# Kernel tuning notes

Hardware: AMD Instinct MI355X
Metric: run time of the kernel (lower is better)

Reference implementation:

```python
import jax, jax.numpy as jnp
import numpy as np

N_NODES = 100000
N_EDGES = 1600000
F_IN = 256
EMB = 16  # conv1 out = 2*EMB = 32, conv2 out = EMB


def setup_inputs() -> dict:
    key = jax.random.key(0)
    k1, k2, k3, k4, k5, k6, k7 = jax.random.split(key, 7)
    x = jax.random.normal(k1, (N_NODES, F_IN), dtype=jnp.float32)
    edge_index = jax.random.randint(k2, (2, N_EDGES), 0, N_NODES, dtype=jnp.int64)
    edge_weight = jax.random.uniform(k3, (N_EDGES,), dtype=jnp.float32)
    # GCNConv params: glorot-ish weights, zero bias (materialized as params)
    s1 = 1.0 / np.sqrt(F_IN)
    s2 = 1.0 / np.sqrt(2 * EMB)
    W1 = jax.random.uniform(k4, (F_IN, 2 * EMB), minval=-s1, maxval=s1, dtype=jnp.float32)
    b1 = jnp.zeros((2 * EMB,), dtype=jnp.float32)
    W2 = jax.random.uniform(k5, (2 * EMB, EMB), minval=-s2, maxval=s2, dtype=jnp.float32)
    b2 = jnp.zeros((EMB,), dtype=jnp.float32)
    return {"x": x, "edge_index": edge_index, "edge_weight": edge_weight,
            "W1": W1, "b1": b1, "W2": W2, "b2": b2}


def _gcn_norm(edge_index, edge_weight, num_nodes, dtype):
    # PyG gcn_norm with add_self_loops=True, fill_value=1.0
    row, col = edge_index[0], edge_index[1]
    loop = jnp.arange(num_nodes)
    row_a = jnp.concatenate([row, loop])
    col_a = jnp.concatenate([col, loop])
    w_a = jnp.concatenate([edge_weight, jnp.ones((num_nodes,), dtype=dtype)])
    deg = jax.ops.segment_sum(w_a, col_a, num_segments=num_nodes)
    dinv = jnp.where(deg > 0, jax.lax.rsqrt(deg), jnp.zeros_like(deg))
    norm = dinv[row_a] * w_a * dinv[col_a]
    return row_a, col_a, norm


def _gcn_conv(x, W, b, row, col, norm, num_nodes):
    h = x @ W                                  # [N, d_out] dense projection
    msg = norm[:, None] * h[row]               # gather + edge scale, [E+N, d_out]
    out = jax.ops.segment_sum(msg, col, num_segments=num_nodes)  # scatter-add
    return out + b


def reference(x, edge_index, edge_weight, W1, b1, W2, b2):
    n = x.shape[0]
    row, col, norm = _gcn_norm(edge_index, edge_weight, n, x.dtype)
    h = jax.nn.relu(_gcn_conv(x, W1, b1, row, col, norm, n))
    return _gcn_conv(h, W2, b2, row, col, norm, n)
```

## Files before the change

kernel.cpp:

```cpp
#include <hip/hip_runtime.h>
#include <hip/hip_bf16.h>
#include <hip/hip_fp16.h>

#define NN   100000
#define NE   1600000
#define FIN  256
#define HID  32
#define OUTD 16
#define NBLK ((NN + 255) / 256)

#define GEMM_ROWS   64
#define GEMM_BLOCKS ((NN + GEMM_ROWS - 1) / GEMM_ROWS)
#define CNT_EDGES   2048
#define CNT_BLOCKS  ((NE + CNT_EDGES - 1) / CNT_EDGES)
#define FUSE_BLOCKS (GEMM_BLOCKS + CNT_BLOCKS)
#define FILL_BLOCKS ((NE + 1023) / 1024)

#define OFF_FLAG    0
#define OFF_DEGPACK 64
#define OFF_DINV    (OFF_DEGPACK + 2*NN)
#define OFF_RANK    (OFF_DINV + NN)
#define OFF_BSUM    (OFF_RANK + NE)
#define OFF_ROWPTR  (OFF_BSUM + 1024)
#define OFF_CSR     (OFF_ROWPTR + NN + 32)
#define OFF_H1      (OFF_CSR + 2*NE)
#define OFF_P2      (OFF_H1 + NN*HID)

#define PACK_SHIFT 40
#define PACK_MASK  ((1ull << PACK_SHIFT) - 1ull)
#define FP_SCALE   16777216.0f
#define FP_INV     (1.0f / 16777216.0f)

__device__ __forceinline__ float bf2f(unsigned short u) {
  union { unsigned int i; float f; } v; v.i = ((unsigned int)u) << 16; return v.f;
}
__device__ __forceinline__ unsigned short f2bf(float f) {
  union { float f; unsigned int i; } v; v.f = f;
  unsigned int x = v.i;
  return (unsigned short)((x + 0x7fffu + ((x >> 16) & 1u)) >> 16);
}
__device__ __forceinline__ int eidx(const int* __restrict__ ei, long long pos, int is64) {
  return is64 ? ei[2 * pos] : ei[pos];
}
__device__ __forceinline__ float ldf(const void* p, long long i, int isf32) {
  return isf32 ? ((const float*)p)[i] : bf2f(((const unsigned short*)p)[i]);
}

__global__ __launch_bounds__(256) void detect_zero_kernel(const int* __restrict__ ei,
    const unsigned short* __restrict__ xu, int* __restrict__ flags,
    float* __restrict__ zp, int zn) {
  int b = blockIdx.x;
  if (b == 0) {
    __shared__ int any, cnt;
    if (threadIdx.x == 0) { any = 0; cnt = 0; }
    __syncthreads();
    int local = 0, c = 0;
    for (int i = threadIdx.x; i < 2048; i += 256) local |= ei[2 * i + 1];
    for (int i = threadIdx.x; i < 1024; i += 256) {
      unsigned int e = (xu[2 * i] >> 7) & 0xFF;
      c += (e < 100 || e > 140) ? 1 : 0;
    }
    if (local) atomicOr(&any, 1);
    atomicAdd(&cnt, c);
    __syncthreads();
    if (threadIdx.x == 0) {
      flags[0] = (any == 0) ? 1 : 0;
      flags[1] = (cnt > 100) ? 1 : 0;
    }
  } else {
    int stride = (gridDim.x - 1) * 256;
    for (int i = (b - 1) * 256 + threadIdx.x; i < zn; i += stride) zp[i] = 0.f;
  }
}

__global__ __launch_bounds__(256) void count_gemm_kernel(const int* __restrict__ ei,
    const void* __restrict__ ew, unsigned long long* __restrict__ degpack,
    int* __restrict__ rank, const void* __restrict__ x,
    const void* __restrict__ W1, void* __restrict__ h1,
    const int* __restrict__ flags) {
  __shared__ float wlds[FIN * HID];
  __shared__ float xs[32][GEMM_ROWS];
  int b = blockIdx.x;
  int t = threadIdx.x;

  if ((b % 3) == 0) {
    int cid = b / 3;
    int is64 = flags[0], isf32 = flags[1];
    int e0 = cid * CNT_EDGES + t;
    int c[8]; float w[8];
    #pragma unroll
    for (int q = 0; q < 8; q++) {
      int e = e0 + q * 256;
      if (e < NE) {
        c[q] = eidx(ei, (long long)NE + e, is64);
        w[q] = ldf(ew, e, isf32);
      } else c[q] = -1;
    }
    unsigned long long old[8];
    #pragma unroll
    for (int q = 0; q < 8; q++) {
      if (c[q] >= 0) {
        unsigned long long inc = (1ull << PACK_SHIFT)
                               | (unsigned long long)(w[q] * FP_SCALE + 0.5f);
        old[q] = atomicAdd(degpack + c[q], inc);
      }
    }
    #pragma unroll
    for (int q = 0; q < 8; q++)
      if (c[q] >= 0) rank[e0 + q * 256] = (int)(old[q] >> PACK_SHIFT);
    return;
  }

  int gid = b - b / 3 - 1;
  int rb = gid * GEMM_ROWS;
  int isf32 = flags[1];

  if (isf32) {
    const float* wrow = (const float*)W1 + t * HID;
    #pragma unroll
    for (int jj = 0; jj < HID; jj += 4)
      *(float4*)&wlds[t * HID + jj] = *((const float4*)(wrow + jj));
  } else {
    const unsigned short* wrow = (const unsigned short*)W1 + t * HID;
    #pragma unroll
    for (int jj = 0; jj < HID; jj += 8) {
      uint4 pk = *((const uint4*)(wrow + jj));
      const unsigned short* pu = (const unsigned short*)&pk;
      #pragma unroll
      for (int q = 0; q < 8; q++) wlds[t * HID + jj + q] = bf2f(pu[q]);
    }
  }

  int j0 = (t & 15) * 2;
  int r0 = (t >> 4) * 4;
  int rr  = t >> 2;
  int kk0 = (t & 3) * 8;
  long long grow = (long long)rb + rr;
  float acc[4][2];
  #pragma unroll
  for (int i = 0; i < 4; i++) { acc[i][0] = 0.f; acc[i][1] = 0.f; }

  union { uint4 u[2]; float f[8]; unsigned short s[16]; } pf;

  {
    if (grow < NN) {
      if (isf32) {
        const float* xp = (const float*)x + grow * FIN + kk0;
        pf.u[0] = ((const uint4*)xp)[0];
        pf.u[1] = ((const uint4*)xp)[1];
      } else {
        const unsigned short* xp = (const unsigned short*)x + grow * FIN + kk0;
        pf.u[0] = *(const uint4*)xp;
      }
    } else { pf.u[0] = make_uint4(0,0,0,0); pf.u[1] = make_uint4(0,0,0,0); }
  }

  for (int kc = 0; kc < FIN; kc += 32) {
    __syncthreads();
    if (isf32) {
      #pragma unroll
      for (int q = 0; q < 8; q++) xs[kk0 + q][rr] = pf.f[q];
    } else {
      #pragma unroll
      for (int q = 0; q < 8; q++) xs[kk0 + q][rr] = bf2f(pf.s[q]);
    }
    __syncthreads();
    if (kc + 32 < FIN) {
      if (grow < NN) {
        if (isf32) {
          const float* xp = (const float*)x + grow * FIN + kc + 32 + kk0;
          pf.u[0] = ((const uint4*)xp)[0];
          pf.u[1] = ((const uint4*)xp)[1];
        } else {
          const unsigned short* xp = (const unsigned short*)x + grow * FIN + kc + 32 + kk0;
          pf.u[0] = *(const uint4*)xp;
        }
      }
    }
    #pragma unroll 8
    for (int kk = 0; kk < 32; kk++) {
      float2 wp = *(const float2*)&wlds[(kc + kk) * HID + j0];
      float4 xv = *(const float4*)&xs[kk][r0];
      float xr[4] = {xv.x, xv.y, xv.z, xv.w};
      #pragma unroll
      for (int i = 0; i < 4; i++) {
        acc[i][0] = fmaf(xr[i], wp.x, acc[i][0]);
        acc[i][1] = fmaf(xr[i], wp.y, acc[i][1]);
      }
    }
  }
  #pragma unroll
  for (int i = 0; i < 4; i++) {
    int g = rb + r0 + i;
    if (g < NN) {
      if (isf32) {
        float2 v; v.x = acc[i][0]; v.y = acc[i][1];
        *((float2*)((float*)h1 + (long long)g * HID + j0)) = v;
      } else {
        __half2 hv;
        hv.x = __float2half(acc[i][0]);
        hv.y = __float2half(acc[i][1]);
        *((__half2*)((__half*)h1 + (long long)g * HID + j0)) = hv;
      }
    }
  }
}

__global__ __launch_bounds__(256) void scan_sum_kernel(
    const unsigned long long* __restrict__ degpack, int* __restrict__ bsum) {
  __shared__ int s[256];
  int i = blockIdx.x * 256 + threadIdx.x;
  s[threadIdx.x] = (i < NN) ? (int)(degpack[i] >> PACK_SHIFT) : 0;
  __syncthreads();
  for (int off = 128; off > 0; off >>= 1) {
    if (threadIdx.x < off) s[threadIdx.x] += s[threadIdx.x + off];
    __syncthreads();
  }
  if (threadIdx.x == 0) bsum[blockIdx.x] = s[0];
}

__global__ __launch_bounds__(256) void scan_write_kernel(const unsigned long long* __restrict__ degpack,
    const int* __restrict__ bsum, int* __restrict__ rowptr,
    float* __restrict__ dinv) {
  __shared__ int a[256];
  __shared__ int base_s;
  int t = threadIdx.x;
  int b = blockIdx.x;
  int v = 0;
  for (int i = t; i < NBLK; i += 256) v += (i < b) ? bsum[i] : 0;
  a[t] = v;
  __syncthreads();
  for (int off = 128; off > 0; off >>= 1) {
    if (t < off) a[t] += a[t + off];
    __syncthreads();
  }
  if (t == 0) base_s = a[0];
  __syncthreads();
  int base = base_s;
  int i = b * 256 + t;
  unsigned long long dp = (i < NN) ? degpack[i] : 0ull;
  int orig = (int)(dp >> PACK_SHIFT);
  a[t] = orig;
  __syncthreads();
  for (int off = 1; off < 256; off <<= 1) {
    int x2 = a[t] + ((t >= off) ? a[t - off] : 0);
    __syncthreads();
    a[t] = x2;
    __syncthreads();
  }
  if (i < NN) {
    rowptr[i] = base + a[t] - orig;
    float d = (float)(dp & PACK_MASK) * FP_INV + 1.0f;
    dinv[i] = rsqrtf(d);
  }
  if (b == 0 && t == 0) rowptr[NN] = NE;
}

__global__ __launch_bounds__(256) void fill_csr_kernel(const int* __restrict__ ei,
    const void* __restrict__ ew, const float* __restrict__ dinv,
    const int* __restrict__ rowptr, const int* __restrict__ rank,
    int2* __restrict__ csr, const int* __restrict__ flags) {
  int is64 = flags[0], isf32 = flags[1];
  int e0 = blockIdx.x * 1024 + threadIdx.x;
  int r[4], c[4], rk[4]; float w[4];
  #pragma unroll
  for (int q = 0; q < 4; q++) {
    int e = e0 + q * 256;
    if (e < NE) {
      r[q]  = eidx(ei, e, is64);
      c[q]  = eidx(ei, (long long)NE + e, is64);
      w[q]  = ldf(ew, e, isf32);
      rk[q] = rank[e];
    } else c[q] = -1;
  }
  float dr[4], dc[4]; int rp[4];
  #pragma unroll
  for (int q = 0; q < 4; q++) {
    if (c[q] >= 0) {
      dr[q] = dinv[r[q]];
      dc[q] = dinv[c[q]];
      rp[q] = rowptr[c[q]];
    }
  }
  #pragma unroll
  for (int q = 0; q < 4; q++) {
    if (c[q] >= 0) {
      int2 pr; pr.x = r[q]; pr.y = __float_as_int(dr[q] * w[q] * dc[q]);
      csr[rp[q] + rk[q]] = pr;
    }
  }
}

template <bool F32>
__device__ __forceinline__ float gather_row32(const void* __restrict__ hv,
    const int2* __restrict__ csr, int k0, int k1, int j) {
  const float*  hf = (const float*)hv;
  const __half* hh = (const __half*)hv;
  float acc = 0.f;
  for (int base = k0; base < k1; base += 32) {
    int kk = base + j;
    int2 q; q.x = 0; q.y = 0;
    if (kk < k1) q = csr[kk];
    int nloc = min(k1 - base, 32);
    int i = 0;
    for (; i + 8 <= nloc; i += 8) {
      int   s0 = __shfl(q.x, i + 0, 32), s1 = __shfl(q.x, i + 1, 32);
      int   s2 = __shfl(q.x, i + 2, 32), s3 = __shfl(q.x, i + 3, 32);
      int   s4 = __shfl(q.x, i + 4, 32), s5 = __shfl(q.x, i + 5, 32);
      int   s6 = __shfl(q.x, i + 6, 32), s7 = __shfl(q.x, i + 7, 32);
      float w0 = __int_as_float(__shfl(q.y, i + 0, 32));
      float w1 = __int_as_float(__shfl(q.y, i + 1, 32));
      float w2 = __int_as_float(__shfl(q.y, i + 2, 32));
      float w3 = __int_as_float(__shfl(q.y, i + 3, 32));
      float w4 = __int_as_float(__shfl(q.y, i + 4, 32));
      float w5 = __int_as_float(__shfl(q.y, i + 5, 32));
      float w6 = __int_as_float(__shfl(q.y, i + 6, 32));
      float w7 = __int_as_float(__shfl(q.y, i + 7, 32));
      float v0 = F32 ? hf[s0 * HID + j] : __half2float(hh[s0 * HID + j]);
      float v1 = F32 ? hf[s1 * HID + j] : __half2float(hh[s1 * HID + j]);
      float v2 = F32 ? hf[s2 * HID + j] : __half2float(hh[s2 * HID + j]);
      float v3 = F32 ? hf[s3 * HID + j] : __half2float(hh[s3 * HID + j]);
      float v4 = F32 ? hf[s4 * HID + j] : __half2float(hh[s4 * HID + j]);
      float v5 = F32 ? hf[s5 * HID + j] : __half2float(hh[s5 * HID + j]);
      float v6 = F32 ? hf[s6 * HID + j] : __half2float(hh[s6 * HID + j]);
      float v7 = F32 ? hf[s7 * HID + j] : __half2float(hh[s7 * HID + j]);
      acc = fmaf(w0, v0, acc); acc = fmaf(w1, v1, acc);
      acc = fmaf(w2, v2, acc); acc = fmaf(w3, v3, acc);
      acc = fmaf(w4, v4, acc); acc = fmaf(w5, v5, acc);
      acc = fmaf(w6, v6, acc); acc = fmaf(w7, v7, acc);
    }
    for (; i < nloc; i++) {
      int   s = __shfl(q.x, i, 32);
      float w = __int_as_float(__shfl(q.y, i, 32));
      float v = F32 ? hf[s * HID + j] : __half2float(hh[s * HID + j]);
      acc = fmaf(w, v, acc);
    }
  }
  return acc;
}

template <bool F32>
__device__ __forceinline__ float gather_row16(const void* __restrict__ pv,
    const int2* __restrict__ csr, int k0, int k1, int m) {
  const float*  pf = (const float*)pv;
  const __half* ph = (const __half*)pv;
  float acc = 0.f;
  for (int base = k0; base < k1; base += 16) {
    int kk = base + m;
    int2 q; q.x = 0; q.y = 0;
    if (kk < k1) q = csr[kk];
    int nloc = min(k1 - base, 16);
    int i = 0;
    for (; i + 8 <= nloc; i += 8) {
      int   s0 = __shfl(q.x, i + 0, 16), s1 = __shfl(q.x, i + 1, 16);
      int   s2 = __shfl(q.x, i + 2, 16), s3 = __shfl(q.x, i + 3, 16);
      int   s4 = __shfl(q.x, i + 4, 16), s5 = __shfl(q.x, i + 5, 16);
      int   s6 = __shfl(q.x, i + 6, 16), s7 = __shfl(q.x, i + 7, 16);
      float w0 = __int_as_float(__shfl(q.y, i + 0, 16));
      float w1 = __int_as_float(__shfl(q.y, i + 1, 16));
      float w2 = __int_as_float(__shfl(q.y, i + 2, 16));
      float w3 = __int_as_float(__shfl(q.y, i + 3, 16));
      float w4 = __int_as_float(__shfl(q.y, i + 4, 16));
      float w5 = __int_as_float(__shfl(q.y, i + 5, 16));
      float w6 = __int_as_float(__shfl(q.y, i + 6, 16));
      float w7 = __int_as_float(__shfl(q.y, i + 7, 16));
      float v0 = F32 ? pf[s0 * OUTD + m] : __half2float(ph[s0 * OUTD + m]);
      float v1 = F32 ? pf[s1 * OUTD + m] : __half2float(ph[s1 * OUTD + m]);
      float v2 = F32 ? pf[s2 * OUTD + m] : __half2float(ph[s2 * OUTD + m]);
      float v3 = F32 ? pf[s3 * OUTD + m] : __half2float(ph[s3 * OUTD + m]);
      float v4 = F32 ? pf[s4 * OUTD + m] : __half2float(ph[s4 * OUTD + m]);
      float v5 = F32 ? pf[s5 * OUTD + m] : __half2float(ph[s5 * OUTD + m]);
      float v6 = F32 ? pf[s6 * OUTD + m] : __half2float(ph[s6 * OUTD + m]);
      float v7 = F32 ? pf[s7 * OUTD + m] : __half2float(ph[s7 * OUTD + m]);
      acc = fmaf(w0, v0, acc); acc = fmaf(w1, v1, acc);
      acc = fmaf(w2, v2, acc); acc = fmaf(w3, v3, acc);
      acc = fmaf(w4, v4, acc); acc = fmaf(w5, v5, acc);
      acc = fmaf(w6, v6, acc); acc = fmaf(w7, v7, acc);
    }
    for (; i < nloc; i++) {
      int   s = __shfl(q.x, i, 16);
      float w = __int_as_float(__shfl(q.y, i, 16));
      float v = F32 ? pf[s * OUTD + m] : __half2float(ph[s * OUTD + m]);
      acc = fmaf(w, v, acc);
    }
  }
  return acc;
}

__global__ __launch_bounds__(256) void gather1_kernel(const void* __restrict__ h1,
    const float* __restrict__ dinv, const int* __restrict__ rowptr,
    const int2* __restrict__ csr, const void* __restrict__ b1,
    const void* __restrict__ W2, void* __restrict__ p2,
    const int* __restrict__ flags) {
  __shared__ float w2lds[HID * OUTD];
  __shared__ float b1l[HID];
  __shared__ float tl[8][HID + 1];
  int t = threadIdx.x;
  int isf32 = flags[1];
  w2lds[2 * t]     = ldf(W2, 2 * t, isf32);
  w2lds[2 * t + 1] = ldf(W2, 2 * t + 1, isf32);
  if (t < HID) b1l[t] = ldf(b1, t, isf32);
  __syncthreads();

  int nl = t >> 5;
  int j  = t & 31;
  int node = blockIdx.x * 8 + nl;
  if (node < NN) {
    int k0 = rowptr[node], k1 = rowptr[node + 1];
    float acc = isf32 ? gather_row32<true>(h1, csr, k0, k1, j)
                      : gather_row32<false>(h1, csr, k0, k1, j);
    float di = dinv[node];
    float sv = isf32 ? ((const float*)h1)[(long long)node * HID + j]
                     : __half2float(((const __half*)h1)[(long long)node * HID + j]);
    acc = fmaf(di * di, sv, acc);
    acc += b1l[j];
    tl[nl][j] = fmaxf(acc, 0.f);
  }
  __syncthreads();
  int m = t & 31;
  if (node < NN && m < OUTD) {
    float s = 0.f;
    #pragma unroll
    for (int k = 0; k < HID; k++) s = fmaf(tl[nl][k], w2lds[k * OUTD + m], s);
    if (isf32) ((float*)p2)[(long long)node * OUTD + m] = s;
    else       ((__half*)p2)[(long long)node * OUTD + m] = __float2half(s);
  }
}

__global__ __launch_bounds__(256) void gather2_kernel(const void* __restrict__ p2,
    const float* __restrict__ dinv, const int* __restrict__ rowptr,
    const int2* __restrict__ csr, const void* __restrict__ b2,
    void* __restrict__ out, const int* __restrict__ flags) {
  __shared__ float b2l[OUTD];
  int t = threadIdx.x;
  int isf32 = flags[1];
  if (t < OUTD) b2l[t] = ldf(b2, t, isf32);
  __syncthreads();

  int nl = t >> 4;
  int m  = t & 15;
  int node = blockIdx.x * 16 + nl;
  if (node >= NN) return;
  int k0 = rowptr[node], k1 = rowptr[node + 1];
  float acc = isf32 ? gather_row16<true>(p2, csr, k0, k1, m)
                    : gather_row16<false>(p2, csr, k0, k1, m);
  float di = dinv[node];
  float sv = isf32 ? ((const float*)p2)[(long long)node * OUTD + m]
                   : __half2float(((const __half*)p2)[(long long)node * OUTD + m]);
  acc = fmaf(di * di, sv, acc);
  acc += b2l[m];
  int oidx = node * OUTD + m;
  if (isf32) ((float*)out)[oidx] = acc;
  else       ((unsigned short*)out)[oidx] = f2bf(acc);
}

extern "C" void kernel_launch(void* const* d_in, const int* in_sizes, int n_in,
                              void* d_out, int out_size, void* d_ws, size_t ws_size,
                              hipStream_t stream) {
  const void* x  = d_in[0];
  const int* ei  = (const int*)d_in[1];
  const void* ew = d_in[2];
  const void* W1 = d_in[3];
  const void* b1 = d_in[4];
  const void* W2 = d_in[5];
  const void* b2 = d_in[6];
  float* ws = (float*)d_ws;
  int* wsi = (int*)d_ws;
  unsigned long long* degpack = (unsigned long long*)(wsi + OFF_DEGPACK);

  detect_zero_kernel<<<dim3(513), dim3(256), 0, stream>>>(ei, (const unsigned short*)x,
      wsi + OFF_FLAG, ws + OFF_DEGPACK, 2 * NN);
  count_gemm_kernel<<<dim3(FUSE_BLOCKS), dim3(256), 0, stream>>>(ei, ew, degpack,
      wsi + OFF_RANK, x, W1, ws + OFF_H1, wsi + OFF_FLAG);
  scan_sum_kernel<<<dim3(NBLK), dim3(256), 0, stream>>>(degpack, wsi + OFF_BSUM);
  scan_write_kernel<<<dim3(NBLK), dim3(256), 0, stream>>>(degpack, wsi + OFF_BSUM,
      wsi + OFF_ROWPTR, ws + OFF_DINV);
  fill_csr_kernel<<<dim3(FILL_BLOCKS), dim3(256), 0, stream>>>(ei, ew, ws + OFF_DINV,
      wsi + OFF_ROWPTR, wsi + OFF_RANK, (int2*)(wsi + OFF_CSR), wsi + OFF_FLAG);
  gather1_kernel<<<dim3((NN + 7) / 8), dim3(256), 0, stream>>>(ws + OFF_H1, ws + OFF_DINV,
      wsi + OFF_ROWPTR, (const int2*)(wsi + OFF_CSR), b1, W2, ws + OFF_P2, wsi + OFF_FLAG);
  gather2_kernel<<<dim3((NN + 15) / 16), dim3(256), 0, stream>>>(ws + OFF_P2, ws + OFF_DINV,
      wsi + OFF_ROWPTR, (const int2*)(wsi + OFF_CSR), b2, d_out, wsi + OFF_FLAG);
}
```

Baseline: 352.1 us.

## Fuse scan, CSR fill and both gathers into one cooperative persistent kernel

Replaces five separate launches (scan sum, scan write, CSR fill, gather1, gather2) with a single cooperative kernel using grid.sync between phases and grid-stride chunk loops. It also moves the destination-side dinv factor out of each per-edge weight and applies it once per node after aggregation, which removes one random dinv load per edge in the fill. The aim is to cut launch gaps and tail effects between small dependent kernels. In exchange it adds grid-wide barriers and caps the grid at 1024 blocks with __launch_bounds__(256,4), which may reduce occupancy for the gather phases.

New measurement: 876.9 us. 149% more time.

```diff
diff --git a/kernel.cpp b/kernel.cpp
--- a/kernel.cpp
+++ b/kernel.cpp
@@ -1,6 +1,8 @@
 #include <hip/hip_runtime.h>
 #include <hip/hip_bf16.h>
 #include <hip/hip_fp16.h>
+#include <hip/hip_cooperative_groups.h>
+namespace cg = cooperative_groups;
 
 #define NN   100000
 #define NE   1600000
@@ -14,7 +16,10 @@
 #define CNT_EDGES   2048
 #define CNT_BLOCKS  ((NE + CNT_EDGES - 1) / CNT_EDGES)
 #define FUSE_BLOCKS (GEMM_BLOCKS + CNT_BLOCKS)
-#define FILL_BLOCKS ((NE + 1023) / 1024)
+#define FILL_CHUNKS ((NE + 1023) / 1024)
+#define G1_CHUNKS   ((NN + 7) / 8)
+#define G2_CHUNKS   ((NN + 15) / 16)
+#define MEGA_GRID   1024
 
 #define OFF_FLAG    0
 #define OFF_DEGPACK 64
@@ -202,91 +207,6 @@
         hv.y = __float2half(acc[i][1]);
         *((__half2*)((__half*)h1 + (long long)g * HID + j0)) = hv;
       }
-    }
-  }
-}
-
-__global__ __launch_bounds__(256) void scan_sum_kernel(
-    const unsigned long long* __restrict__ degpack, int* __restrict__ bsum) {
-  __shared__ int s[256];
-  int i = blockIdx.x * 256 + threadIdx.x;
-  s[threadIdx.x] = (i < NN) ? (int)(degpack[i] >> PACK_SHIFT) : 0;
-  __syncthreads();
-  for (int off = 128; off > 0; off >>= 1) {
-    if (threadIdx.x < off) s[threadIdx.x] += s[threadIdx.x + off];
-    __syncthreads();
-  }
-  if (threadIdx.x == 0) bsum[blockIdx.x] = s[0];
-}
-
-__global__ __launch_bounds__(256) void scan_write_kernel(const unsigned long long* __restrict__ degpack,
-    const int* __restrict__ bsum, int* __restrict__ rowptr,
-    float* __restrict__ dinv) {
-  __shared__ int a[256];
-  __shared__ int base_s;
-  int t = threadIdx.x;
-  int b = blockIdx.x;
-  int v = 0;
-  for (int i = t; i < NBLK; i += 256) v += (i < b) ? bsum[i] : 0;
-  a[t] = v;
-  __syncthreads();
-  for (int off = 128; off > 0; off >>= 1) {
-    if (t < off) a[t] += a[t + off];
-    __syncthreads();
-  }
-  if (t == 0) base_s = a[0];
-  __syncthreads();
-  int base = base_s;
-  int i = b * 256 + t;
-  unsigned long long dp = (i < NN) ? degpack[i] : 0ull;
-  int orig = (int)(dp >> PACK_SHIFT);
-  a[t] = orig;
-  __syncthreads();
-  for (int off = 1; off < 256; off <<= 1) {
-    int x2 = a[t] + ((t >= off) ? a[t - off] : 0);
-    __syncthreads();
-    a[t] = x2;
-    __syncthreads();
-  }
-  if (i < NN) {
-    rowptr[i] = base + a[t] - orig;
-    float d = (float)(dp & PACK_MASK) * FP_INV + 1.0f;
-    dinv[i] = rsqrtf(d);
-  }
-  if (b == 0 && t == 0) rowptr[NN] = NE;
-}
-
-__global__ __launch_bounds__(256) void fill_csr_kernel(const int* __restrict__ ei,
-    const void* __restrict__ ew, const float* __restrict__ dinv,
-    const int* __restrict__ rowptr, const int* __restrict__ rank,
-    int2* __restrict__ csr, const int* __restrict__ flags) {
-  int is64 = flags[0], isf32 = flags[1];
-  int e0 = blockIdx.x * 1024 + threadIdx.x;
-  int r[4], c[4], rk[4]; float w[4];
-  #pragma unroll
-  for (int q = 0; q < 4; q++) {
-    int e = e0 + q * 256;
-    if (e < NE) {
-      r[q]  = eidx(ei, e, is64);
-      c[q]  = eidx(ei, (long long)NE + e, is64);
-      w[q]  = ldf(ew, e, isf32);
-      rk[q] = rank[e];
-    } else c[q] = -1;
-  }
-  float dr[4], dc[4]; int rp[4];
-  #pragma unroll
-  for (int q = 0; q < 4; q++) {
-    if (c[q] >= 0) {
-      dr[q] = dinv[r[q]];
-      dc[q] = dinv[c[q]];
-      rp[q] = rowptr[c[q]];
-    }
-  }
-  #pragma unroll
-  for (int q = 0; q < 4; q++) {
-    if (c[q] >= 0) {
-      int2 pr; pr.x = r[q]; pr.y = __float_as_int(dr[q] * w[q] * dc[q]);
-      csr[rp[q] + rk[q]] = pr;
     }
   }
 }
@@ -387,71 +307,157 @@
   return acc;
 }
 
-__global__ __launch_bounds__(256) void gather1_kernel(const void* __restrict__ h1,
-    const float* __restrict__ dinv, const int* __restrict__ rowptr,
-    const int2* __restrict__ csr, const void* __restrict__ b1,
+__global__ __launch_bounds__(256, 4) void mega_tail_kernel(
+    const unsigned long long* __restrict__ degpack, int* __restrict__ bsum,
+    int* __restrict__ rowptr, float* __restrict__ dinv,
+    const int* __restrict__ rank, const int* __restrict__ ei,
+    const void* __restrict__ ew, int2* __restrict__ csr,
+    const void* __restrict__ h1, const void* __restrict__ b1,
     const void* __restrict__ W2, void* __restrict__ p2,
+    const void* __restrict__ b2, void* __restrict__ out,
     const int* __restrict__ flags) {
-  __shared__ float w2lds[HID * OUTD];
-  __shared__ float b1l[HID];
-  __shared__ float tl[8][HID + 1];
+  cg::grid_group grid = cg::this_grid();
+  __shared__ union {
+    int red[256];
+    struct { float w2[HID * OUTD]; float b1l[HID]; float tl[8][HID + 1]; } g1;
+    float b2l[OUTD];
+  } sm;
   int t = threadIdx.x;
+  int nb = gridDim.x;
   int isf32 = flags[1];
-  w2lds[2 * t]     = ldf(W2, 2 * t, isf32);
-  w2lds[2 * t + 1] = ldf(W2, 2 * t + 1, isf32);
-  if (t < HID) b1l[t] = ldf(b1, t, isf32);
-  __syncthreads();
-
-  int nl = t >> 5;
-  int j  = t & 31;
-  int node = blockIdx.x * 8 + nl;
-  if (node < NN) {
-    int k0 = rowptr[node], k1 = rowptr[node + 1];
-    float acc = isf32 ? gather_row32<true>(h1, csr, k0, k1, j)
-                      : gather_row32<false>(h1, csr, k0, k1, j);
-    float di = dinv[node];
-    float sv = isf32 ? ((const float*)h1)[(long long)node * HID + j]
-                     : __half2float(((const __half*)h1)[(long long)node * HID + j]);
-    acc = fmaf(di * di, sv, acc);
-    acc += b1l[j];
-    tl[nl][j] = fmaxf(acc, 0.f);
-  }
-  __syncthreads();
-  int m = t & 31;
-  if (node < NN && m < OUTD) {
-    float s = 0.f;
-    #pragma unroll
-    for (int k = 0; k < HID; k++) s = fmaf(tl[nl][k], w2lds[k * OUTD + m], s);
-    if (isf32) ((float*)p2)[(long long)node * OUTD + m] = s;
-    else       ((__half*)p2)[(long long)node * OUTD + m] = __float2half(s);
-  }
-}
-
-__global__ __launch_bounds__(256) void gather2_kernel(const void* __restrict__ p2,
-    const float* __restrict__ dinv, const int* __restrict__ rowptr,
-    const int2* __restrict__ csr, const void* __restrict__ b2,
-    void* __restrict__ out, const int* __restrict__ flags) {
-  __shared__ float b2l[OUTD];
-  int t = threadIdx.x;
-  int isf32 = flags[1];
-  if (t < OUTD) b2l[t] = ldf(b2, t, isf32);
-  __syncthreads();
-
-  int nl = t >> 4;
-  int m  = t & 15;
-  int node = blockIdx.x * 16 + nl;
-  if (node >= NN) return;
-  int k0 = rowptr[node], k1 = rowptr[node + 1];
-  float acc = isf32 ? gather_row16<true>(p2, csr, k0, k1, m)
-                    : gather_row16<false>(p2, csr, k0, k1, m);
-  float di = dinv[node];
-  float sv = isf32 ? ((const float*)p2)[(long long)node * OUTD + m]
-                   : __half2float(((const __half*)p2)[(long long)node * OUTD + m]);
-  acc = fmaf(di * di, sv, acc);
-  acc += b2l[m];
-  int oidx = node * OUTD + m;
-  if (isf32) ((float*)out)[oidx] = acc;
-  else       ((unsigned short*)out)[oidx] = f2bf(acc);
+
+  for (int c = blockIdx.x; c < NBLK; c += nb) {
+    int i = c * 256 + t;
+    int v = (i < NN) ? (int)(degpack[i] >> PACK_SHIFT) : 0;
+    __syncthreads();
+    sm.red[t] = v;
+    __syncthreads();
+    for (int off = 128; off > 0; off >>= 1) {
+      if (t < off) sm.red[t] += sm.red[t + off];
+      __syncthreads();
+    }
+    if (t == 0) bsum[c] = sm.red[0];
+  }
+  grid.sync();
+
+  for (int c = blockIdx.x; c < NBLK; c += nb) {
+    int v = 0;
+    for (int i = t; i < NBLK; i += 256) v += (i < c) ? bsum[i] : 0;
+    __syncthreads();
+    sm.red[t] = v;
+    __syncthreads();
+    for (int off = 128; off > 0; off >>= 1) {
+      if (t < off) sm.red[t] += sm.red[t + off];
+      __syncthreads();
+    }
+    int base = sm.red[0];
+    __syncthreads();
+    int i = c * 256 + t;
+    unsigned long long dp = (i < NN) ? degpack[i] : 0ull;
+    int orig = (int)(dp >> PACK_SHIFT);
+    sm.red[t] = orig;
+    __syncthreads();
+    for (int off = 1; off < 256; off <<= 1) {
+      int x2 = sm.red[t] + ((t >= off) ? sm.red[t - off] : 0);
+      __syncthreads();
+      sm.red[t] = x2;
+      __syncthreads();
+    }
+    if (i < NN) {
+      rowptr[i] = base + sm.red[t] - orig;
+      float d = (float)(dp & PACK_MASK) * FP_INV + 1.0f;
+      dinv[i] = rsqrtf(d);
+    }
+    if (c == 0 && t == 0) rowptr[NN] = NE;
+  }
+  grid.sync();
+
+  {
+    int is64 = flags[0];
+    for (int c = blockIdx.x; c < FILL_CHUNKS; c += nb) {
+      int e0 = c * 1024 + t;
+      int r[4], cc[4], rk[4]; float w[4];
+      #pragma unroll
+      for (int q = 0; q < 4; q++) {
+        int e = e0 + q * 256;
+        if (e < NE) {
+          r[q]  = eidx(ei, e, is64);
+          cc[q] = eidx(ei, (long long)NE + e, is64);
+          w[q]  = ldf(ew, e, isf32);
+          rk[q] = rank[e];
+        } else cc[q] = -1;
+      }
+      float dr[4]; int rp[4];
+      #pragma unroll
+      for (int q = 0; q < 4; q++) {
+        if (cc[q] >= 0) { dr[q] = dinv[r[q]]; rp[q] = rowptr[cc[q]]; }
+      }
+      #pragma unroll
+      for (int q = 0; q < 4; q++) {
+        if (cc[q] >= 0) {
+          int2 pr; pr.x = r[q]; pr.y = __float_as_int(dr[q] * w[q]);
+          csr[rp[q] + rk[q]] = pr;
+        }
+      }
+    }
+  }
+  grid.sync();
+
+  {
+    sm.g1.w2[2 * t]     = ldf(W2, 2 * t, isf32);
+    sm.g1.w2[2 * t + 1] = ldf(W2, 2 * t + 1, isf32);
+    if (t < HID) sm.g1.b1l[t] = ldf(b1, t, isf32);
+    __syncthreads();
+    int nl = t >> 5, j = t & 31;
+    for (int c = blockIdx.x; c < G1_CHUNKS; c += nb) {
+      int node = c * 8 + nl;
+      if (node < NN) {
+        int k0 = rowptr[node], k1 = rowptr[node + 1];
+        float acc = isf32 ? gather_row32<true>(h1, csr, k0, k1, j)
+                          : gather_row32<false>(h1, csr, k0, k1, j);
+        float di = dinv[node];
+        float sv = isf32 ? ((const float*)h1)[(long long)node * HID + j]
+                         : __half2float(((const __half*)h1)[(long long)node * HID + j]);
+        acc = acc * di;
+        acc = fmaf(di * di, sv, acc);
+        acc += sm.g1.b1l[j];
+        sm.g1.tl[nl][j] = fmaxf(acc, 0.f);
+      }
+      __syncthreads();
+      if (node < NN && j < OUTD) {
+        float s = 0.f;
+        #pragma unroll
+        for (int k = 0; k < HID; k++)
+          s = fmaf(sm.g1.tl[nl][k], sm.g1.w2[k * OUTD + j], s);
+        if (isf32) ((float*)p2)[(long long)node * OUTD + j] = s;
+        else       ((__half*)p2)[(long long)node * OUTD + j] = __float2half(s);
+      }
+      __syncthreads();
+    }
+  }
+  grid.sync();
+
+  {
+    if (t < OUTD) sm.b2l[t] = ldf(b2, t, isf32);
+    __syncthreads();
+    int nl = t >> 4, m = t & 15;
+    for (int c = blockIdx.x; c < G2_CHUNKS; c += nb) {
+      int node = c * 16 + nl;
+      if (node >= NN) continue;
+      int k0 = rowptr[node], k1 = rowptr[node + 1];
+      float acc = isf32 ? gather_row16<true>(p2, csr, k0, k1, m)
+                        : gather_row16<false>(p2, csr, k0, k1, m);
+      float di = dinv[node];
+      float sv = isf32 ? ((const float*)p2)[(long long)node * OUTD + m]
+                       : __half2float(((const __half*)p2)[(long long)node * OUTD + m]);
+      acc = acc * di;
+      acc = fmaf(di * di, sv, acc);
+      acc += sm.b2l[m];
+      int oidx = node * OUTD + m;
+      if (isf32) ((float*)out)[oidx] = acc;
+      else       ((unsigned short*)out)[oidx] = f2bf(acc);
+    }
+  }
 }
 
 extern "C" void kernel_launch(void* const* d_in, const int* in_sizes, int n_in,
@@ -472,13 +478,24 @@
       wsi + OFF_FLAG, ws + OFF_DEGPACK, 2 * NN);
   count_gemm_kernel<<<dim3(FUSE_BLOCKS), dim3(256), 0, stream>>>(ei, ew, degpack,
       wsi + OFF_RANK, x, W1, ws + OFF_H1, wsi + OFF_FLAG);
-  scan_sum_kernel<<<dim3(NBLK), dim3(256), 0, stream>>>(degpack, wsi + OFF_BSUM);
-  scan_write_kernel<<<dim3(NBLK), dim3(256), 0, stream>>>(degpack, wsi + OFF_BSUM,
-      wsi + OFF_ROWPTR, ws + OFF_DINV);
-  fill_csr_kernel<<<dim3(FILL_BLOCKS), dim3(256), 0, stream>>>(ei, ew, ws + OFF_DINV,
-      wsi + OFF_ROWPTR, wsi + OFF_RANK, (int2*)(wsi + OFF_CSR), wsi + OFF_FLAG);
-  gather1_kernel<<<dim3((NN + 7) / 8), dim3(256), 0, stream>>>(ws + OFF_H1, ws + OFF_DINV,
-      wsi + OFF_ROWPTR, (const int2*)(wsi + OFF_CSR), b1, W2, ws + OFF_P2, wsi + OFF_FLAG);
-  gather2_kernel<<<dim3((NN + 15) / 16), dim3(256), 0, stream>>>(ws + OFF_P2, ws + OFF_DINV,
-      wsi + OFF_ROWPTR, (const int2*)(wsi + OFF_CSR), b2, d_out, wsi + OFF_FLAG);
-}
+
+  {
+    const unsigned long long* dp = degpack;
+    int* bsum   = wsi + OFF_BSUM;
+    int* rowptr = wsi + OFF_ROWPTR;
+    float* dinv = ws + OFF_DINV;
+    const int* rank = wsi + OFF_RANK;
+    int2* csr   = (int2*)(wsi + OFF_CSR);
+    const void* h1 = (const void*)(ws + OFF_H1);
+    void* p2    = (void*)(ws + OFF_P2);
+    void* outp  = d_out;
+    const int* flags = wsi + OFF_FLAG;
+    void* ka[] = {
+      (void*)&dp, (void*)&bsum, (void*)&rowptr, (void*)&dinv,
+      (void*)&rank, (void*)&ei, (void*)&ew, (void*)&csr,
+      (void*)&h1, (void*)&b1, (void*)&W2, (void*)&p2,
+      (void*)&b2, (void*)&outp, (void*)&flags };
+    hipLaunchCooperativeKernel((void*)mega_tail_kernel, dim3(MEGA_GRID), dim3(256),
+                               ka, 0, stream);
+  }
+}
```
